# Optimization experiments

Hardware: AMD Instinct MI355X
Metric: run time of the kernel (lower is better)

## Reference

```python
import jax, jax.numpy as jnp
from jax import lax
import numpy as np

B, HI, WI = 8, 56, 56
HO, WO = HI // 2, WI // 2
DIN, DOUT = 96, 192
N_IN, N_OUT = HI * WI, HO * WO
HD = 32
NH = DOUT // HD
H2, W2, N2 = HO, WO, HO * WO
NA_W = 7
NUM_ITERS, DEPTH = 3, 2


def _build_group_tables():
    # M_loc: 0 inside 3x3 output window around each input token, -1e4 elsewhere
    # qidx: which of the 9 relative offsets maps (input i -> output j); -1 outside window
    mask = np.full((N_IN, N_OUT), -1e4, np.float32)
    idx = np.full((N_IN, N_OUT), -1, np.int64)
    rr, cc = np.meshgrid(np.arange(HI), np.arange(WI), indexing='ij')
    rr, cc = rr.ravel(), cc.ravel()
    r0, c0 = rr // 2, cc // 2
    ii = np.arange(N_IN)
    offs = [(dr, dc) for dr in (-1, 0, 1) for dc in (-1, 0, 1)]
    for kk, (dr, dc) in enumerate(offs):
        oi = np.clip(r0 + dr, 0, HO - 1) * WO + np.clip(c0 + dc, 0, WO - 1)
        mask[ii, oi] = 0.0
        idx[ii, oi] = kk
    # torch rpb[-1] == rpb[8]; emulate negative indexing with %9
    return jnp.asarray(mask), jnp.asarray(idx % 9)

M_LOC, QIDX = _build_group_tables()


def _rope_tables(n, d):
    inv = 1.0 / (10000.0 ** (np.arange(0, d, 2, dtype=np.float32) / d))
    ang = np.outer(np.arange(n, dtype=np.float32), inv)
    return jnp.asarray(np.cos(ang), jnp.float32), jnp.asarray(np.sin(ang), jnp.float32)

ROPE_COS, ROPE_SIN = _rope_tables(N2, HD)


def _na_idx(n, w):
    # NATTEN-style shifted windows: center clamped so the window stays in-bounds
    half = w // 2
    c = np.clip(np.arange(n), half, n - 1 - half)
    return jnp.asarray(c[:, None] + np.arange(-half, half + 1)[None, :])

NB_R = _na_idx(H2, NA_W)
NB_C = _na_idx(W2, NA_W)


def _ln(x, g, b):
    m = x.mean(-1, keepdims=True)
    v = ((x - m) ** 2).mean(-1, keepdims=True)
    return (x - m) / jnp.sqrt(v + 1e-5) * g + b


def _rope(t):  # t: [B, N, heads, head_dim]
    b, n, h, d = t.shape
    tr = t.reshape(b, n, h, d // 2, 2)
    x0, x1 = tr[..., 0], tr[..., 1]
    c = ROPE_COS[None, :, None, :]
    s = ROPE_SIN[None, :, None, :]
    return jnp.stack([x0 * c - x1 * s, x1 * c + x0 * s], -1).reshape(b, n, h, d)


def _forward(x, seed_conv_w, q_proj_w, k_proj_w, v_proj_w, g_ln_in_g, g_ln_in_b, g_ln_out_g, g_ln_out_b, g_ln_attn_g, g_ln_attn_b, g_ln_mlp_g, g_ln_mlp_b, g_mlp_w1, g_mlp_b1, g_mlp_w2, g_mlp_b2, tau, rpb, blk_ln1_g, blk_ln1_b, blk_ln2_g, blk_ln2_b, blk_qkv_w, blk_proj_w, blk_proj_b, blk_mlp_w1, blk_mlp_b1, blk_mlp_w2, blk_mlp_b2):
    b = x.shape[0]
    # ---- SparseGroupingLayer (local/sparse path), eval mode ----
    xc = x.transpose(0, 2, 1).reshape(b, DIN, HI, WI)
    seed = lax.conv_general_dilated(xc, seed_conv_w, (2, 2), ((1, 1), (1, 1)), dimension_numbers=('NCHW', 'OIHW', 'NCHW'))
    x_out = _ln(seed.reshape(b, DOUT, N_OUT).transpose(0, 2, 1), g_ln_out_g, g_ln_out_b)
    xn = _ln(x, g_ln_in_g, g_ln_in_b)
    k = xn @ k_proj_w.T
    v = xn @ v_proj_w.T
    bias = rpb[QIDX] + M_LOC  # [N_in, N_out]
    scale = jnp.exp(tau[0])
    for _ in range(NUM_ITERS):
        q = _ln(x_out, g_ln_out_g, g_ln_out_b) @ q_proj_w.T  # [B, N_out, dim_in]
        logits = jnp.einsum('bnd,bmd->bnm', k, q) * scale + bias[None]
        a_ups = jax.nn.softmax(logits, -1)
        a_down = a_ups / (a_ups.sum(1, keepdims=True) + 1e-8)
        upd = jnp.einsum('bnm,bnd->bmd', a_down, v)
        x_out = x_out + _ln(upd, g_ln_attn_g, g_ln_attn_b)
        h = jax.nn.gelu(x_out @ g_mlp_w1.T + g_mlp_b1, approximate=False) @ g_mlp_w2.T + g_mlp_b2
        x_out = x_out + _ln(h, g_ln_mlp_g, g_ln_mlp_b)
    # ---- SeNaTraBlocks: neighborhood attention (window=7) + RoPE, eval mode ----
    rows = NB_R[:, None, :, None]
    cols = NB_C[None, :, None, :]
    for i in range(DEPTH):
        xb = _ln(x_out, blk_ln1_g[i], blk_ln1_b[i])
        qkv = (xb @ blk_qkv_w[i].T).reshape(b, N2, 3, NH, HD)
        q = _rope(qkv[:, :, 0]).transpose(0, 2, 1, 3).reshape(b, NH, H2, W2, HD)
        kk = _rope(qkv[:, :, 1]).transpose(0, 2, 1, 3).reshape(b, NH, H2, W2, HD)
        vv = qkv[:, :, 2].transpose(0, 2, 1, 3).reshape(b, NH, H2, W2, HD)
        kn = kk[:, :, rows, cols].reshape(b, NH, H2, W2, NA_W * NA_W, HD)
        vn = vv[:, :, rows, cols].reshape(b, NH, H2, W2, NA_W * NA_W, HD)
        att = jnp.einsum('bhijd,bhijkd->bhijk', q, kn) * (HD ** -0.5)
        att = jax.nn.softmax(att, -1)
        o = jnp.einsum('bhijk,bhijkd->bhijd', att, vn)
        o = o.reshape(b, NH, N2, HD).transpose(0, 2, 1, 3).reshape(b, N2, DOUT)
        x_out = x_out + (o @ blk_proj_w[i].T + blk_proj_b[i])
        xb = _ln(x_out, blk_ln2_g[i], blk_ln2_b[i])
        h = jax.nn.gelu(xb @ blk_mlp_w1[i].T + blk_mlp_b1[i], approximate=False) @ blk_mlp_w2[i].T + blk_mlp_b2[i]
        x_out = x_out + h
    return x_out


def setup_inputs() -> dict:
    key = jax.random.key(0)
    ks = jax.random.split(key, 12)
    hid_g, hid_b = 2 * DOUT, 3 * DOUT
    def rn(k, shape, s=0.02):
        return jax.random.normal(k, shape, jnp.float32) * s
    return {
        'x': jax.random.normal(ks[0], (B, N_IN, DIN), jnp.float32),
        'seed_conv_w': rn(ks[1], (DOUT, DIN, 3, 3), 0.05),
        'q_proj_w': rn(ks[2], (DIN, DOUT)),
        'k_proj_w': rn(ks[3], (DIN, DIN)),
        'v_proj_w': rn(ks[4], (DOUT, DIN)),
        'g_ln_in_g': jnp.ones((DIN,), jnp.float32), 'g_ln_in_b': jnp.zeros((DIN,), jnp.float32),
        'g_ln_out_g': jnp.ones((DOUT,), jnp.float32), 'g_ln_out_b': jnp.zeros((DOUT,), jnp.float32),
        'g_ln_attn_g': jnp.ones((DOUT,), jnp.float32), 'g_ln_attn_b': jnp.zeros((DOUT,), jnp.float32),
        'g_ln_mlp_g': jnp.ones((DOUT,), jnp.float32), 'g_ln_mlp_b': jnp.zeros((DOUT,), jnp.float32),
        'g_mlp_w1': rn(ks[5], (hid_g, DOUT)), 'g_mlp_b1': jnp.zeros((hid_g,), jnp.float32),
        'g_mlp_w2': rn(ks[6], (DOUT, hid_g)), 'g_mlp_b2': jnp.zeros((DOUT,), jnp.float32),
        'tau': jnp.array([float(np.log(DIN ** -0.5))], jnp.float32),
        'rpb': rn(ks[7], (9,)),
        'blk_ln1_g': jnp.ones((DEPTH, DOUT), jnp.float32), 'blk_ln1_b': jnp.zeros((DEPTH, DOUT), jnp.float32),
        'blk_ln2_g': jnp.ones((DEPTH, DOUT), jnp.float32), 'blk_ln2_b': jnp.zeros((DEPTH, DOUT), jnp.float32),
        'blk_qkv_w': rn(ks[8], (DEPTH, 3 * DOUT, DOUT)),
        'blk_proj_w': rn(ks[9], (DEPTH, DOUT, DOUT)), 'blk_proj_b': jnp.zeros((DEPTH, DOUT), jnp.float32),
        'blk_mlp_w1': rn(ks[10], (DEPTH, hid_b, DOUT)), 'blk_mlp_b1': jnp.zeros((DEPTH, hid_b), jnp.float32),
        'blk_mlp_w2': rn(ks[11], (DEPTH, DOUT, hid_b)), 'blk_mlp_b2': jnp.zeros((DEPTH, DOUT), jnp.float32),
    }


def reference(x, seed_conv_w, q_proj_w, k_proj_w, v_proj_w, g_ln_in_g, g_ln_in_b, g_ln_out_g, g_ln_out_b, g_ln_attn_g, g_ln_attn_b, g_ln_mlp_g, g_ln_mlp_b, g_mlp_w1, g_mlp_b1, g_mlp_w2, g_mlp_b2, tau, rpb, blk_ln1_g, blk_ln1_b, blk_ln2_g, blk_ln2_b, blk_qkv_w, blk_proj_w, blk_proj_b, blk_mlp_w1, blk_mlp_b1, blk_mlp_w2, blk_mlp_b2):
    return _forward(x, seed_conv_w, q_proj_w, k_proj_w, v_proj_w, g_ln_in_g, g_ln_in_b, g_ln_out_g, g_ln_out_b, g_ln_attn_g, g_ln_attn_b, g_ln_mlp_g, g_ln_mlp_b, g_mlp_w1, g_mlp_b1, g_mlp_w2, g_mlp_b2, tau, rpb, blk_ln1_g, blk_ln1_b, blk_ln2_g, blk_ln2_b, blk_qkv_w, blk_proj_w, blk_proj_b, blk_mlp_w1, blk_mlp_b1, blk_mlp_w2, blk_mlp_b2)
```

## Files before the change

kernel.cpp:

```cpp
#include <hip/hip_runtime.h>
#include <hip/hip_bf16.h>

#define DEV __device__ __forceinline__

typedef __attribute__((ext_vector_type(8))) short short8;
typedef __attribute__((ext_vector_type(4))) float f32x4;

DEV unsigned short f2b(float f) {
  union { float f; unsigned u; } v; v.f = f;
  unsigned r = v.u + 0x7FFFu + ((v.u >> 16) & 1u);
  return (unsigned short)(r >> 16);
}
DEV float b2f16(unsigned short b) {
  union { unsigned u; float f; } v; v.u = ((unsigned)b) << 16;
  return v.f;
}
DEV void tsplit(float v, short& h, short& l) {
  union { float f; unsigned u; } c; c.f = v;
  unsigned short hu = (unsigned short)(c.u >> 16);
  union { unsigned u; float f; } hb; hb.u = (unsigned)hu << 16;
  union { float f; unsigned u; } c2; c2.f = v - hb.f;
  h = (short)hu; l = (short)(c2.u >> 16);
}

__global__ void k_castw(const float* __restrict__ s0, const float* __restrict__ s1,
    const float* __restrict__ s2, const float* __restrict__ s3,
    const float* __restrict__ s4, const float* __restrict__ s5,
    const float* __restrict__ s6, const float* __restrict__ s7,
    const float* __restrict__ s8, const float* __restrict__ s9,
    short* __restrict__ dh, short* __restrict__ dl) {
  int idx = blockIdx.x * 256 + threadIdx.x;
  if (idx >= 1096704) return;
  float v;
  if (idx < 165888) {
    int co = idx / 864, rem = idx % 864;
    int k9 = rem / 96, ci = rem % 96;
    v = s0[co * 864 + ci * 9 + k9];
  } else {
    const float* src; int base;
    if      (idx < 175104) { src = s1; base = 165888; }
    else if (idx < 193536) { src = s2; base = 175104; }
    else if (idx < 211968) { src = s3; base = 193536; }
    else if (idx < 285696) { src = s4; base = 211968; }
    else if (idx < 359424) { src = s5; base = 285696; }
    else if (idx < 580608) { src = s6; base = 359424; }
    else if (idx < 654336) { src = s7; base = 580608; }
    else if (idx < 875520) { src = s8; base = 654336; }
    else                   { src = s9; base = 875520; }
    v = src[idx - base];
  }
  unsigned short h = f2b(v);
  dh[idx] = (short)h;
  dl[idx] = (short)f2b(v - b2f16(h));
}

__global__ void k_rope(float* ct, float* st) {
  int idx = blockIdx.x * 256 + threadIdx.x;
  if (idx >= 784 * 16) return;
  int n = idx >> 4, j = idx & 15;
  float inv = powf(10000.f, -(float)(2 * j) / 32.f);
  float ang = (float)n * inv;
  ct[idx] = cosf(ang);
  st[idx] = sinf(ang);
}

template<int D>
__global__ __launch_bounds__(256) void k_lnstat(const float* __restrict__ in,
    float2* __restrict__ stats, int M) {
  int tok = blockIdx.x * 4 + (threadIdx.x >> 6);
  int l = threadIdx.x & 63;
  if (tok >= M) return;
  const float* row = in + (size_t)tok * D;
  constexpr int E = (D + 63) / 64;
  float s = 0.f, s2 = 0.f;
#pragma unroll
  for (int e = 0; e < E; ++e) {
    int i = e * 64 + l;
    float x = (i < D) ? row[i] : 0.f;
    s += x; s2 += x * x;
  }
  for (int off = 32; off; off >>= 1) { s += __shfl_xor(s, off); s2 += __shfl_xor(s2, off); }
  float mean = s / D, var = s2 / D - mean * mean;
  if (l == 0) stats[tok] = make_float2(mean, rsqrtf(var + 1e-5f));
}

template<int ADD>
__global__ __launch_bounds__(256) void k_ln_epi(const float* __restrict__ raw,
    const float* __restrict__ g, const float* __restrict__ b,
    float* __restrict__ out, float2* __restrict__ stats, int M) {
  int tok = blockIdx.x * 4 + (threadIdx.x >> 6);
  int l = threadIdx.x & 63;
  if (tok >= M) return;
  const float* row = raw + (size_t)tok * 192;
  float v[3];
  float s = 0.f, s2 = 0.f;
#pragma unroll
  for (int e = 0; e < 3; ++e) {
    float x = row[e * 64 + l];
    v[e] = x; s += x; s2 += x * x;
  }
  for (int off = 32; off; off >>= 1) { s += __shfl_xor(s, off); s2 += __shfl_xor(s2, off); }
  float mean = s / 192.f, var = s2 / 192.f - mean * mean;
  float rstd = rsqrtf(var + 1e-5f);
  float* orow = out + (size_t)tok * 192;
  float t = 0.f, t2 = 0.f;
#pragma unroll
  for (int e = 0; e < 3; ++e) {
    int i = e * 64 + l;
    float r = (v[e] - mean) * rstd * g[i] + b[i];
    float nv = ADD ? (orow[i] + r) : r;
    orow[i] = nv;
    t += nv; t2 += nv * nv;
  }
  for (int off = 32; off; off >>= 1) { t += __shfl_xor(t, off); t2 += __shfl_xor(t2, off); }
  float m2 = t / 192.f, v2 = t2 / 192.f - m2 * m2;
  if (l == 0) stats[tok] = make_float2(m2, rsqrtf(v2 + 1e-5f));
}

template<int EPI, int CONV, int LNS>
__global__ __launch_bounds__(256) void k_mgemm(
    const float* __restrict__ A, const short* __restrict__ WH,
    const short* __restrict__ WL, const float* __restrict__ bias,
    float* __restrict__ C, int M, int N, int K,
    const float2* __restrict__ lnstats, const float* __restrict__ lng,
    const float* __restrict__ lnb,
    const float* __restrict__ ct, const float* __restrict__ st,
    float* __restrict__ o1, float* __restrict__ o2, float* __restrict__ o3) {
  __shared__ short AsH[64][40], AsL[64][40];
  __shared__ short BsH[64][40], BsL[64][40];
  int t = threadIdx.x;
  int m0 = blockIdx.x * 64, n0 = blockIdx.y * 64;
  int sr = t >> 2, sq = (t & 3) * 8;
  int lane = t & 63, w = t >> 6, wm = w >> 1, wn = w & 1;
  int fr = lane & 15, fq = lane >> 4;
  float2 lst = make_float2(0.f, 1.f);
  if (LNS) lst = lnstats[m0 + sr];
  f32x4 acc[2][2];
#pragma unroll
  for (int i = 0; i < 2; ++i)
#pragma unroll
    for (int j = 0; j < 2; ++j) acc[i][j] = (f32x4){0.f, 0.f, 0.f, 0.f};

  for (int kt = 0; kt < K; kt += 32) {
    short8 vh, vl;
    if (CONV) {
      int m = m0 + sr;
      int b = m / 784, rm = m % 784, ho = rm / 28, wo = rm % 28;
      int k = kt + sq;
      int k9 = k / 96, ci0 = k % 96;
      int hi = 2 * ho - 1 + k9 / 3, wi = 2 * wo - 1 + k9 % 3;
      if (hi >= 0 && hi < 56 && wi >= 0 && wi < 56) {
        const float* src = &A[((size_t)b * 3136 + hi * 56 + wi) * 96 + ci0];
        float4 a0 = *(const float4*)src;
        float4 a1 = *(const float4*)(src + 4);
        float av[8] = {a0.x, a0.y, a0.z, a0.w, a1.x, a1.y, a1.z, a1.w};
#pragma unroll
        for (int j = 0; j < 8; ++j) { short h, l2; tsplit(av[j], h, l2); vh[j] = h; vl[j] = l2; }
      } else {
#pragma unroll
        for (int j = 0; j < 8; ++j) { vh[j] = 0; vl[j] = 0; }
      }
    } else {
      const float4 a0 = *(const float4*)&A[(size_t)(m0 + sr) * K + kt + sq];
      const float4 a1 = *(const float4*)&A[(size_t)(m0 + sr) * K + kt + sq + 4];
      float av[8] = {a0.x, a0.y, a0.z, a0.w, a1.x, a1.y, a1.z, a1.w};
#pragma unroll
      for (int j = 0; j < 8; ++j) {
        if (LNS) av[j] = (av[j] - lst.x) * lst.y * lng[kt + sq + j] + lnb[kt + sq + j];
        short h, l2; tsplit(av[j], h, l2); vh[j] = h; vl[j] = l2;
      }
    }
    *(short8*)&AsH[sr][sq] = vh;
    *(short8*)&AsL[sr][sq] = vl;
    {
      int n = n0 + sr;
      if (n < N) {
        *(short8*)&BsH[sr][sq] = *(const short8*)&WH[(size_t)n * K + kt + sq];
        *(short8*)&BsL[sr][sq] = *(const short8*)&WL[(size_t)n * K + kt + sq];
      } else {
        short8 z = {0, 0, 0, 0, 0, 0, 0, 0};
        *(short8*)&BsH[sr][sq] = z;
        *(short8*)&BsL[sr][sq] = z;
      }
    }
    __syncthreads();
    short8 ah[2], al[2], bh[2], bl[2];
#pragma unroll
    for (int s = 0; s < 2; ++s) {
      ah[s] = *(const short8*)&AsH[wm * 32 + s * 16 + fr][fq * 8];
      al[s] = *(const short8*)&AsL[wm * 32 + s * 16 + fr][fq * 8];
      bh[s] = *(const short8*)&BsH[wn * 32 + s * 16 + fr][fq * 8];
      bl[s] = *(const short8*)&BsL[wn * 32 + s * 16 + fr][fq * 8];
    }
#pragma unroll
    for (int i = 0; i < 2; ++i)
#pragma unroll
      for (int j = 0; j < 2; ++j) {
        acc[i][j] = __builtin_amdgcn_mfma_f32_16x16x32_bf16(ah[i], bh[j], acc[i][j], 0, 0, 0);
        acc[i][j] = __builtin_amdgcn_mfma_f32_16x16x32_bf16(ah[i], bl[j], acc[i][j], 0, 0, 0);
        acc[i][j] = __builtin_amdgcn_mfma_f32_16x16x32_bf16(al[i], bh[j], acc[i][j], 0, 0, 0);
      }
    __syncthreads();
  }
#pragma unroll
  for (int i = 0; i < 2; ++i) {
#pragma unroll
    for (int j = 0; j < 2; ++j) {
      int n = n0 + wn * 32 + j * 16 + fr;
#pragma unroll
      for (int r = 0; r < 4; ++r) {
        int m = m0 + wm * 32 + i * 16 + fq * 4 + r;
        float v = acc[i][j][r];
        float pa = 0.f;
        if (EPI == 3) pa = __shfl_xor(v, 1);
        if (n >= N) continue;
        if (bias) v += bias[n];
        if (EPI == 1) v = 0.5f * v * (1.f + erff(v * 0.70710678118654752f));
        if (EPI == 3) {
          int sec = n / 192, d = n % 192, h = d / 32, dh = d % 32;
          int b = m / 784, mm = m % 784;
          float val;
          if (sec < 2) {
            int jj = dh >> 1;
            float cc = ct[mm * 16 + jj], ss = st[mm * 16 + jj];
            val = (dh & 1) ? (v * cc + pa * ss) : (v * cc - pa * ss);
          } else val = v;
          float* dst = (sec == 0) ? o1 : ((sec == 1) ? o2 : o3);
          dst[(((size_t)b * 6 + h) * 784 + mm) * 32 + dh] = val;
        } else if (EPI == 2) {
          C[(size_t)m * N + n] += v;
        } else {
          C[(size_t)m * N + n] = v;
        }
      }
      if (EPI == 4 && n < N) {
        int mb = m0 + wm * 32 + i * 16 + fq * 4;
        float4 tv = make_float4(acc[i][j][0], acc[i][j][1], acc[i][j][2], acc[i][j][3]);
        *(float4*)&o1[(size_t)n * M + mb] = tv;
      }
    }
  }
}

__global__ void k_pass1(const float* __restrict__ kkT, const float* __restrict__ q,
    const float* __restrict__ rpb, const float* __restrict__ tau,
    float* __restrict__ M, float* __restrict__ Z) {
  int id = blockIdx.x * 256 + threadIdx.x;
  if (id >= 8 * 3136) return;
  int b = id / 3136, n = id % 3136;
  int r = n / 56, c = n % 56, r0 = r >> 1, c0 = c >> 1;
  int oi[9];
#pragma unroll
  for (int kki = 0; kki < 9; ++kki) {
    int dr = kki / 3 - 1, dc = kki % 3 - 1;
    int rr = min(max(r0 + dr, 0), 27), cc = min(max(c0 + dc, 0), 27);
    oi[kki] = rr * 28 + cc;
  }
  float scale = expf(tau[0]);
  float lg[9]; bool keep[9];
  float mx = -1e30f;
#pragma unroll
  for (int kki = 0; kki < 9; ++kki) {
    bool kp = true;
#pragma unroll
    for (int k2 = kki + 1; k2 < 9; ++k2) if (oi[k2] == oi[kki]) kp = false;
    keep[kki] = kp;
    if (kp) {
      const float* qr = q + ((size_t)b * 784 + oi[kki]) * 96;
      float d = 0.f;
      for (int i = 0; i < 96; ++i) d += kkT[(size_t)i * 25088 + id] * qr[i];
      lg[kki] = d * scale + rpb[kki];
      mx = fmaxf(mx, lg[kki]);
    } else lg[kki] = -1e30f;
  }
  float z = 0.f;
#pragma unroll
  for (int kki = 0; kki < 9; ++kki) if (keep[kki]) z += expf(lg[kki] - mx);
  M[id] = mx; Z[id] = z;
}

__global__ __launch_bounds__(192) void k_pass2(const float* __restrict__ kk,
    const float* __restrict__ q, const float* __restrict__ vv,
    const float* __restrict__ M, const float* __restrict__ Z,
    const float* __restrict__ rpb, const float* __restrict__ tau,
    const float* __restrict__ g, const float* __restrict__ bb, float* __restrict__ xout) {
  int blk = blockIdx.x, b = blk / 784, m = blk % 784;
  int r2 = m / 28, c2 = m % 28;
  int r0lo = (r2 == 0) ? 0 : r2 - 1, r0hi = (r2 == 27) ? 27 : r2 + 1;
  int c0lo = (c2 == 0) ? 0 : c2 - 1, c0hi = (c2 == 27) ? 27 : c2 + 1;
  int nrow = 2 * (r0hi - r0lo + 1), ncol = 2 * (c0hi - c0lo + 1);
  int cnt = nrow * ncol;
  __shared__ float qm[96], p[36];
  __shared__ int nlist[36];
  __shared__ float2 red[192];
  int t = threadIdx.x;
  if (t < 96) qm[t] = q[(size_t)blk * 96 + t];
  __syncthreads();
  if (t < cnt) {
    int rr = 2 * r0lo + t / ncol, cc = 2 * c0lo + t % ncol;
    int n = rr * 56 + cc, rr0 = rr >> 1, cc0 = cc >> 1;
    int kkf = 0;
#pragma unroll
    for (int kki = 0; kki < 9; ++kki) {
      int dr = kki / 3 - 1, dc = kki % 3 - 1;
      int ra = min(max(rr0 + dr, 0), 27), ca = min(max(cc0 + dc, 0), 27);
      if (ra == r2 && ca == c2) kkf = kki;
    }
    const float* krow = kk + ((size_t)b * 3136 + n) * 96;
    float d = 0.f;
    for (int i = 0; i < 96; ++i) d += krow[i] * qm[i];
    float scale = expf(tau[0]);
    float lg = d * scale + rpb[kkf];
    size_t idn = (size_t)b * 3136 + n;
    p[t] = expf(lg - M[idn]) / Z[idn];
    nlist[t] = n;
  }
  __syncthreads();
  float denom = 0.f;
  for (int jn = 0; jn < cnt; ++jn) denom += p[jn];
  float acc = 0.f;
  for (int jn = 0; jn < cnt; ++jn)
    acc += p[jn] * vv[((size_t)b * 3136 + nlist[jn]) * 192 + t];
  float upd = acc / (denom + 1e-8f);
  red[t] = make_float2(upd, upd * upd);
  __syncthreads();
  for (int s = 128; s > 0; s >>= 1) {
    if (t < s && t + s < 192) { red[t].x += red[t + s].x; red[t].y += red[t + s].y; }
    __syncthreads();
  }
  float mean = red[0].x / 192.f, var = red[0].y / 192.f - mean * mean;
  float rstd = rsqrtf(var + 1e-5f);
  xout[(size_t)blk * 192 + t] += (upd - mean) * rstd * g[t] + bb[t];
}

__global__ __launch_bounds__(256) void k_attn(const float* __restrict__ q3,
    const float* __restrict__ k3, const float* __restrict__ v3, float* __restrict__ ob) {
  int bid = blockIdx.x;
  int swz = (bid & 7) * 1176 + (bid >> 3);
  int unit = swz * 4 + (threadIdx.x >> 6);
  int l = threadIdx.x & 63;
  int b = unit / (6 * 784), rem = unit % (6 * 784), h = rem / 784, m = rem % 784;
  int i = m / 28, j = m % 28;
  int ib = min(max(i, 3), 24) - 3, jb = min(max(j, 3), 24) - 3;
  size_t base = (size_t)(b * 6 + h) * 784 * 32;
  const float4* q4 = (const float4*)(q3 + base + (size_t)m * 32);
  float4 qv[8];
#pragma unroll
  for (int e = 0; e < 8; ++e) qv[e] = q4[e];
  float logit = -1e30f;
  if (l < 49) {
    int nk = (ib + l / 7) * 28 + (jb + l % 7);
    const float4* k4 = (const float4*)(k3 + base + (size_t)nk * 32);
    float a = 0.f;
#pragma unroll
    for (int e = 0; e < 8; ++e) {
      float4 kv = k4[e];
      a += qv[e].x * kv.x + qv[e].y * kv.y + qv[e].z * kv.z + qv[e].w * kv.w;
    }
    logit = a * 0.17677669529663687f;
  }
  float mx = logit;
  for (int off = 32; off; off >>= 1) mx = fmaxf(mx, __shfl_xor(mx, off));
  float p = (l < 49) ? expf(logit - mx) : 0.f;
  float sum = p;
  for (int off = 32; off; off >>= 1) sum += __shfl_xor(sum, off);
  int d = l & 31;
  const float* vb = v3 + base + d;
  int rowbase = ib * 28 + jb;
  float acc = 0.f;
  int pbits = __float_as_int(p);
#pragma unroll
  for (int kki = 0; kki < 49; ++kki) {
    float pk = __int_as_float(__builtin_amdgcn_readlane(pbits, kki));
    int nk = rowbase + (kki / 7) * 28 + (kki % 7);
    acc += pk * vb[(size_t)nk * 32];
  }
  if (l < 32)
    ob[(((size_t)b * 784 + m) * 6 + h) * 32 + l] = acc / sum;
}

extern "C" void kernel_launch(void* const* d_in, const int* in_sizes, int n_in,
                              void* d_out, int out_size, void* d_ws, size_t ws_size,
                              hipStream_t stream) {
  (void)in_sizes; (void)n_in; (void)out_size; (void)ws_size;
  const float* x        = (const float*)d_in[0];
  const float* convw    = (const float*)d_in[1];
  const float* qw       = (const float*)d_in[2];
  const float* kw       = (const float*)d_in[3];
  const float* vw       = (const float*)d_in[4];
  const float* ln_in_g  = (const float*)d_in[5];
  const float* ln_in_b  = (const float*)d_in[6];
  const float* ln_out_g = (const float*)d_in[7];
  const float* ln_out_b = (const float*)d_in[8];
  const float* ln_at_g  = (const float*)d_in[9];
  const float* ln_at_b  = (const float*)d_in[10];
  const float* ln_ml_g  = (const float*)d_in[11];
  const float* ln_ml_b  = (const float*)d_in[12];
  const float* gw1      = (const float*)d_in[13];
  const float* gb1      = (const float*)d_in[14];
  const float* gw2      = (const float*)d_in[15];
  const float* gb2      = (const float*)d_in[16];
  const float* tau      = (const float*)d_in[17];
  const float* rpb      = (const float*)d_in[18];
  const float* bln1g    = (const float*)d_in[19];
  const float* bln1b    = (const float*)d_in[20];
  const float* bln2g    = (const float*)d_in[21];
  const float* bln2b    = (const float*)d_in[22];
  const float* bqkvw    = (const float*)d_in[23];
  const float* bprojw   = (const float*)d_in[24];
  const float* bprojb   = (const float*)d_in[25];
  const float* bmw1     = (const float*)d_in[26];
  const float* bmb1     = (const float*)d_in[27];
  const float* bmw2     = (const float*)d_in[28];
  const float* bmb2     = (const float*)d_in[29];

  float* XOUT = (float*)d_out;

  float* W = (float*)d_ws;
  size_t off = 0;
  float* Kb    = W + off; off += (size_t)25088 * 96;
  float* KbT   = W + off; off += (size_t)25088 * 96;
  float* Vb    = W + off; off += (size_t)25088 * 192;
  float* Qb    = W + off; off += (size_t)6272 * 96;
  float* Mb    = W + off; off += (size_t)25088;
  float* Zb    = W + off; off += (size_t)25088;
  float* H1    = W + off; off += (size_t)6272 * 576;
  float* T2    = W + off; off += (size_t)6272 * 192;
  float* CT    = W + off; off += (size_t)784 * 16;
  float* ST    = W + off; off += (size_t)784 * 16;
  float2* S96  = (float2*)(W + off); off += (size_t)25088 * 2;
  float2* S192 = (float2*)(W + off); off += (size_t)6272 * 2;
  short* WBH   = (short*)(W + off); off += (size_t)548352 + 16;
  short* WBL   = (short*)(W + off); off += (size_t)548352 + 16;
  const size_t O_c = 0, O_k = 165888, O_v = 175104, O_q = 193536,
               O_g1 = 211968, O_g2 = 285696, O_qkv = 359424, O_p = 580608,
               O_m1 = 654336, O_m2 = 875520;
  float* CRAW = T2;
  float* Q3 = Kb;
  float* K3 = KbT;
  float* V3 = Vb;
  float* OB = Vb + (size_t)1204224;

  k_castw<<<4284, 256, 0, stream>>>(convw, kw, vw, qw, gw1, gw2, bqkvw, bprojw,
                                    bmw1, bmw2, WBH, WBL);
  k_rope<<<49, 256, 0, stream>>>(CT, ST);

  k_mgemm<0, 1, 0><<<dim3(98, 3), 256, 0, stream>>>(x, WBH + O_c, WBL + O_c, nullptr,
      CRAW, 6272, 192, 864, nullptr, nullptr, nullptr,
      nullptr, nullptr, nullptr, nullptr, nullptr);
  k_ln_epi<0><<<1568, 256, 0, stream>>>(CRAW, ln_out_g, ln_out_b, XOUT, S192, 6272);

  k_lnstat<96><<<6272, 256, 0, stream>>>(x, S96, 25088);
  k_mgemm<4, 0, 1><<<dim3(392, 2), 256, 0, stream>>>(x, WBH + O_k, WBL + O_k, nullptr,
      Kb, 25088, 96, 96, S96, ln_in_g, ln_in_b,
      nullptr, nullptr, KbT, nullptr, nullptr);
  k_mgemm<0, 0, 1><<<dim3(392, 3), 256, 0, stream>>>(x, WBH + O_v, WBL + O_v, nullptr,
      Vb, 25088, 192, 96, S96, ln_in_g, ln_in_b,
      nullptr, nullptr, nullptr, nullptr, nullptr);

  for (int it = 0; it < 3; ++it) {
    k_mgemm<0, 0, 1><<<dim3(98, 2), 256, 0, stream>>>(XOUT, WBH + O_q, WBL + O_q, nullptr,
        Qb, 6272, 96, 192, S192, ln_out_g, ln_out_b,
        nullptr, nullptr, nullptr, nullptr, nullptr);
    k_pass1<<<98, 256, 0, stream>>>(KbT, Qb, rpb, tau, Mb, Zb);
    k_pass2<<<6272, 192, 0, stream>>>(Kb, Qb, Vb, Mb, Zb, rpb, tau, ln_at_g, ln_at_b, XOUT);
    k_mgemm<1, 0, 0><<<dim3(98, 6), 256, 0, stream>>>(XOUT, WBH + O_g1, WBL + O_g1, gb1,
        H1, 6272, 384, 192, nullptr, nullptr, nullptr,
        nullptr, nullptr, nullptr, nullptr, nullptr);
    k_mgemm<0, 0, 0><<<dim3(98, 3), 256, 0, stream>>>(H1, WBH + O_g2, WBL + O_g2, gb2,
        T2, 6272, 192, 384, nullptr, nullptr, nullptr,
        nullptr, nullptr, nullptr, nullptr, nullptr);
    k_ln_epi<1><<<1568, 256, 0, stream>>>(T2, ln_ml_g, ln_ml_b, XOUT, S192, 6272);
  }

  for (int i = 0; i < 2; ++i) {
    if (i == 1) k_lnstat<192><<<1568, 256, 0, stream>>>(XOUT, S192, 6272);
    k_mgemm<3, 0, 1><<<dim3(98, 9), 256, 0, stream>>>(XOUT, WBH + O_qkv + (size_t)i * 110592,
        WBL + O_qkv + (size_t)i * 110592, nullptr,
        nullptr, 6272, 576, 192, S192, bln1g + (size_t)i * 192, bln1b + (size_t)i * 192,
        CT, ST, Q3, K3, V3);
    k_attn<<<9408, 256, 0, stream>>>(Q3, K3, V3, OB);
    k_mgemm<2, 0, 0><<<dim3(98, 3), 256, 0, stream>>>(OB, WBH + O_p + (size_t)i * 36864,
        WBL + O_p + (size_t)i * 36864, bprojb + (size_t)i * 192,
        XOUT, 6272, 192, 192, nullptr, nullptr, nullptr,
        nullptr, nullptr, nullptr, nullptr, nullptr);
    k_lnstat<192><<<1568, 256, 0, stream>>>(XOUT, S192, 6272);
    k_mgemm<1, 0, 1><<<dim3(98, 9), 256, 0, stream>>>(XOUT, WBH + O_m1 + (size_t)i * 110592,
        WBL + O_m1 + (size_t)i * 110592, bmb1 + (size_t)i * 576,
        H1, 6272, 576, 192, S192, bln2g + (size_t)i * 192, bln2b + (size_t)i * 192,
        nullptr, nullptr, nullptr, nullptr, nullptr);
    k_mgemm<2, 0, 0><<<dim3(98, 3), 256, 0, stream>>>(H1, WBH + O_m2 + (size_t)i * 110592,
        WBL + O_m2 + (size_t)i * 110592, bmb2 + (size_t)i * 192,
        XOUT, 6272, 192, 576, nullptr, nullptr, nullptr,
        nullptr, nullptr, nullptr, nullptr, nullptr);
  }
}
```

Measured before the change: 704.4 us.

## Parallelize pass1 with one wavefront per token and split attn PV loop

k_pass1 now assigns a 64-lane wavefront to each input token, with lanes sharing the 96-wide dot products and reducing them by shuffle. The old version ran one thread per token over a transposed K copy on only 98 blocks. This removes the transposed K output from the K GEMM epilogue and frees that buffer. k_attn's 49-term PV accumulation is split across the two 32-lane halves of the wavefront and combined with a shuffle, which halves the serial loop length at the cost of some extra shuffles.

```diff
diff --git a/kernel.cpp b/kernel.cpp
--- a/kernel.cpp
+++ b/kernel.cpp
@@ -233,50 +233,52 @@
           C[(size_t)m * N + n] = v;
         }
       }
-      if (EPI == 4 && n < N) {
-        int mb = m0 + wm * 32 + i * 16 + fq * 4;
-        float4 tv = make_float4(acc[i][j][0], acc[i][j][1], acc[i][j][2], acc[i][j][3]);
-        *(float4*)&o1[(size_t)n * M + mb] = tv;
-      }
     }
   }
 }
 
-__global__ void k_pass1(const float* __restrict__ kkT, const float* __restrict__ q,
-    const float* __restrict__ rpb, const float* __restrict__ tau,
-    float* __restrict__ M, float* __restrict__ Z) {
-  int id = blockIdx.x * 256 + threadIdx.x;
-  if (id >= 8 * 3136) return;
-  int b = id / 3136, n = id % 3136;
+__global__ __launch_bounds__(256) void k_pass1(const float* __restrict__ kk,
+    const float* __restrict__ q, const float* __restrict__ rpb,
+    const float* __restrict__ tau, float* __restrict__ M, float* __restrict__ Z) {
+  int tok = blockIdx.x * 4 + (threadIdx.x >> 6);
+  int l = threadIdx.x & 63;
+  int b = tok / 3136, n = tok % 3136;
   int r = n / 56, c = n % 56, r0 = r >> 1, c0 = c >> 1;
-  int oi[9];
+  int oi[9]; bool keep[9];
 #pragma unroll
   for (int kki = 0; kki < 9; ++kki) {
     int dr = kki / 3 - 1, dc = kki % 3 - 1;
     int rr = min(max(r0 + dr, 0), 27), cc = min(max(c0 + dc, 0), 27);
     oi[kki] = rr * 28 + cc;
   }
-  float scale = expf(tau[0]);
-  float lg[9]; bool keep[9];
-  float mx = -1e30f;
 #pragma unroll
   for (int kki = 0; kki < 9; ++kki) {
     bool kp = true;
 #pragma unroll
     for (int k2 = kki + 1; k2 < 9; ++k2) if (oi[k2] == oi[kki]) kp = false;
     keep[kki] = kp;
-    if (kp) {
+  }
+  float scale = expf(tau[0]);
+  const float* kr = kk + (size_t)tok * 96;
+  float k0 = kr[l];
+  float k1 = (l < 32) ? kr[64 + l] : 0.f;
+  float lg[9];
+  float mx = -1e30f;
+#pragma unroll
+  for (int kki = 0; kki < 9; ++kki) {
+    if (keep[kki]) {
       const float* qr = q + ((size_t)b * 784 + oi[kki]) * 96;
-      float d = 0.f;
-      for (int i = 0; i < 96; ++i) d += kkT[(size_t)i * 25088 + id] * qr[i];
-      lg[kki] = d * scale + rpb[kki];
+      float part = k0 * qr[l];
+      if (l < 32) part += k1 * qr[64 + l];
+      for (int off = 32; off; off >>= 1) part += __shfl_xor(part, off);
+      lg[kki] = part * scale + rpb[kki];
       mx = fmaxf(mx, lg[kki]);
     } else lg[kki] = -1e30f;
   }
   float z = 0.f;
 #pragma unroll
   for (int kki = 0; kki < 9; ++kki) if (keep[kki]) z += expf(lg[kki] - mx);
-  M[id] = mx; Z[id] = z;
+  if (l == 0) { M[tok] = mx; Z[tok] = z; }
 }
 
 __global__ __launch_bounds__(192) void k_pass2(const float* __restrict__ kk,
@@ -364,17 +366,24 @@
   float p = (l < 49) ? expf(logit - mx) : 0.f;
   float sum = p;
   for (int off = 32; off; off >>= 1) sum += __shfl_xor(sum, off);
-  int d = l & 31;
+  int half = l >> 5, d = l & 31;
   const float* vb = v3 + base + d;
   int rowbase = ib * 28 + jb;
   float acc = 0.f;
   int pbits = __float_as_int(p);
 #pragma unroll
-  for (int kki = 0; kki < 49; ++kki) {
-    float pk = __int_as_float(__builtin_amdgcn_readlane(pbits, kki));
-    int nk = rowbase + (kki / 7) * 28 + (kki % 7);
+  for (int kk2 = 0; kk2 < 25; ++kk2) {
+    const int k0c = kk2;
+    const int k1c = (kk2 + 25 <= 48) ? kk2 + 25 : 48;
+    float pk0 = __int_as_float(__builtin_amdgcn_readlane(pbits, k0c));
+    float pk1 = (kk2 < 24) ? __int_as_float(__builtin_amdgcn_readlane(pbits, k1c)) : 0.f;
+    const int c0 = (k0c / 7) * 28 + (k0c % 7);
+    const int c1 = (k1c / 7) * 28 + (k1c % 7);
+    float pk = half ? pk1 : pk0;
+    int nk = rowbase + (half ? c1 : c0);
     acc += pk * vb[(size_t)nk * 32];
   }
+  acc += __shfl_xor(acc, 32);
   if (l < 32)
     ob[(((size_t)b * 784 + m) * 6 + h) * 32 + l] = acc / sum;
 }
@@ -419,7 +428,6 @@
   float* W = (float*)d_ws;
   size_t off = 0;
   float* Kb    = W + off; off += (size_t)25088 * 96;
-  float* KbT   = W + off; off += (size_t)25088 * 96;
   float* Vb    = W + off; off += (size_t)25088 * 192;
   float* Qb    = W + off; off += (size_t)6272 * 96;
   float* Mb    = W + off; off += (size_t)25088;
@@ -437,7 +445,7 @@
                O_m1 = 654336, O_m2 = 875520;
   float* CRAW = T2;
   float* Q3 = Kb;
-  float* K3 = KbT;
+  float* K3 = Kb + (size_t)1204224;
   float* V3 = Vb;
   float* OB = Vb + (size_t)1204224;
 
@@ -451,9 +459,9 @@
   k_ln_epi<0><<<1568, 256, 0, stream>>>(CRAW, ln_out_g, ln_out_b, XOUT, S192, 6272);
 
   k_lnstat<96><<<6272, 256, 0, stream>>>(x, S96, 25088);
-  k_mgemm<4, 0, 1><<<dim3(392, 2), 256, 0, stream>>>(x, WBH + O_k, WBL + O_k, nullptr,
+  k_mgemm<0, 0, 1><<<dim3(392, 2), 256, 0, stream>>>(x, WBH + O_k, WBL + O_k, nullptr,
       Kb, 25088, 96, 96, S96, ln_in_g, ln_in_b,
-      nullptr, nullptr, KbT, nullptr, nullptr);
+      nullptr, nullptr, nullptr, nullptr, nullptr);
   k_mgemm<0, 0, 1><<<dim3(392, 3), 256, 0, stream>>>(x, WBH + O_v, WBL + O_v, nullptr,
       Vb, 25088, 192, 96, S96, ln_in_g, ln_in_b,
       nullptr, nullptr, nullptr, nullptr, nullptr);
@@ -462,7 +470,7 @@
     k_mgemm<0, 0, 1><<<dim3(98, 2), 256, 0, stream>>>(XOUT, WBH + O_q, WBL + O_q, nullptr,
         Qb, 6272, 96, 192, S192, ln_out_g, ln_out_b,
         nullptr, nullptr, nullptr, nullptr, nullptr);
-    k_pass1<<<98, 256, 0, stream>>>(KbT, Qb, rpb, tau, Mb, Zb);
+    k_pass1<<<6272, 256, 0, stream>>>(Kb, Qb, rpb, tau, Mb, Zb);
     k_pass2<<<6272, 192, 0, stream>>>(Kb, Qb, Vb, Mb, Zb, rpb, tau, ln_at_g, ln_at_b, XOUT);
     k_mgemm<1, 0, 0><<<dim3(98, 6), 256, 0, stream>>>(XOUT, WBH + O_g1, WBL + O_g1, gb1,
         H1, 6272, 384, 192, nullptr, nullptr, nullptr,
```

Result: faster. 654.7 us (-7.0%).
